# Performance work log

Hardware: AMD Instinct MI355X
Metric: run time of the kernel (lower is better)

## Reference

```python
import jax, jax.numpy as jnp
import numpy as np

C = 512
NUM_HEADS = 8
HEAD_DIM = C // NUM_HEADS  # 64
BN_EPS = 1e-5


def setup_inputs() -> dict:
    key = jax.random.key(0)
    ks = jax.random.split(key, 12)
    B, H, W = 8, 32, 32
    s = 0.02
    return {
        "x": jax.random.normal(ks[0], (B, C, H, W), dtype=jnp.float32),
        "gamma": jnp.ones((C,), jnp.float32),
        "beta": jnp.zeros((C,), jnp.float32),
        "rmean": jnp.zeros((C,), jnp.float32),
        "rvar": jnp.ones((C,), jnp.float32),
        "wq": jax.random.normal(ks[1], (C, C), jnp.float32) * s,
        "bq": jnp.zeros((C,), jnp.float32),
        "wk": jax.random.normal(ks[2], (C, C), jnp.float32) * s,
        "bk": jnp.zeros((C,), jnp.float32),
        "wv": jax.random.normal(ks[3], (C, C), jnp.float32) * s,
        "bv": jnp.zeros((C,), jnp.float32),
        "wp": jax.random.normal(ks[4], (C, C), jnp.float32) * s,
        "bp": jnp.zeros((C,), jnp.float32),
    }


def _conv1x1(w, b, h):
    # 1x1 conv == per-pixel dense: (O,C) x (B,C,H,W) -> (B,O,H,W)
    return jnp.einsum('oc,bchw->bohw', w, h) + b[None, :, None, None]


def reference(x, gamma, beta, rmean, rvar, wq, bq, wk, bk, wv, bv, wp, bp):
    B, Cc, H, W = x.shape
    N = H * W
    # BatchNorm2d (eval mode, running stats)
    inv = gamma / jnp.sqrt(rvar + BN_EPS)
    h = x * inv[None, :, None, None] + (beta - rmean * inv)[None, :, None, None]
    q = _conv1x1(wq, bq, h).reshape(B, NUM_HEADS, HEAD_DIM, N)
    k = _conv1x1(wk, bk, h).reshape(B, NUM_HEADS, HEAD_DIM, N)
    v = _conv1x1(wv, bv, h).reshape(B, NUM_HEADS, HEAD_DIM, N)
    scale = 1.0 / np.sqrt(HEAD_DIM).astype(np.float32)
    attn = jnp.einsum('bhdn,bhdm->bhnm', q, k) * scale  # [B,heads,N,N]
    attn = jnp.clip(attn, -50.0, 50.0)
    attn = jax.nn.softmax(attn, axis=-1)
    out = jnp.einsum('bhnm,bhdm->bhdn', attn, v).reshape(B, Cc, H, W)
    out = _conv1x1(wp, bp, out)
    return x + out
```

## Files before the change

kernel.cpp:

```cpp
#include <hip/hip_runtime.h>
#include <stdint.h>

#define C_DIM 512
#define NHEADS 8
#define HDIM 64
#define BATCH 8
#define NPIX 1024
#define Q_PRESCALE 0.18033688011112042f

typedef __bf16 bf16x8 __attribute__((ext_vector_type(8)));
typedef float f32x4 __attribute__((ext_vector_type(4)));
typedef float f32x16 __attribute__((ext_vector_type(16)));

__device__ __forceinline__ unsigned short f2bf(float f) {
  union { float f; unsigned u; } v; v.f = f;
  unsigned r = v.u + 0x7fffu + ((v.u >> 16) & 1u);
  return (unsigned short)(r >> 16);
}

__device__ __forceinline__ void gl_lds16(const void* g, void* l) {
  __builtin_amdgcn_global_load_lds(
      (__attribute__((address_space(1))) void*)g,
      (__attribute__((address_space(3))) void*)l,
      16, 0, 0);
}

__global__ __launch_bounds__(256) void k_prep(const float* __restrict__ wq,
                                              const float* __restrict__ wk,
                                              const float* __restrict__ wv,
                                              const float* __restrict__ wp,
                                              unsigned short* __restrict__ wbf) {
  const int n = C_DIM * C_DIM;
  for (int i = blockIdx.x * blockDim.x + threadIdx.x; i < 4 * n;
       i += gridDim.x * blockDim.x) {
    const float* src = (i < n) ? wq : (i < 2 * n) ? wk : (i < 3 * n) ? wv : wp;
    wbf[i] = f2bf(src[i & (n - 1)]);
  }
}

__global__ __launch_bounds__(256) void k_bnT(const float* __restrict__ x,
                                             const float* __restrict__ gamma,
                                             const float* __restrict__ beta,
                                             const float* __restrict__ rmean,
                                             const float* __restrict__ rvar,
                                             unsigned short* __restrict__ hbT) {
  __shared__ unsigned short tile[64][72];
  const int b = blockIdx.z, c0 = blockIdx.y * 64, n0 = blockIdx.x * 64;
  const int t = threadIdx.x;
#pragma unroll
  for (int it = 0; it < 4; ++it) {
    int c = it * 16 + (t >> 4);
    int n = (t & 15) * 4;
    const float4 v = *(const float4*)&x[((size_t)b * C_DIM + c0 + c) * NPIX + n0 + n];
    int cc = c0 + c;
    float inv = gamma[cc] * rsqrtf(rvar[cc] + 1e-5f);
    float add = beta[cc] - rmean[cc] * inv;
    tile[c][n + 0] = f2bf(v.x * inv + add);
    tile[c][n + 1] = f2bf(v.y * inv + add);
    tile[c][n + 2] = f2bf(v.z * inv + add);
    tile[c][n + 3] = f2bf(v.w * inv + add);
  }
  __syncthreads();
#pragma unroll
  for (int it = 0; it < 2; ++it) {
    int n = it * 32 + (t >> 3);
    int cj = (t & 7) * 8;
    unsigned short tmp[8];
#pragma unroll
    for (int u = 0; u < 8; ++u) tmp[u] = tile[cj + u][n];
    uint4 pk;
    pk.x = (unsigned)tmp[0] | ((unsigned)tmp[1] << 16);
    pk.y = (unsigned)tmp[2] | ((unsigned)tmp[3] << 16);
    pk.z = (unsigned)tmp[4] | ((unsigned)tmp[5] << 16);
    pk.w = (unsigned)tmp[6] | ((unsigned)tmp[7] << 16);
    *(uint4*)&hbT[((size_t)b * NPIX + n0 + n) * C_DIM + c0 + cj] = pk;
  }
}

__global__ __launch_bounds__(256) void k_qkv(const unsigned short* __restrict__ wbf,
                                             const float* __restrict__ bq,
                                             const float* __restrict__ bk,
                                             const float* __restrict__ bv,
                                             const unsigned short* __restrict__ hbT,
                                             unsigned short* __restrict__ QT,
                                             unsigned short* __restrict__ KT,
                                             unsigned short* __restrict__ Vb) {
  __shared__ unsigned short Atile[128 * 32];
  __shared__ unsigned short Btile[128 * 32];
  const int which = blockIdx.z >> 3;
  const int b = blockIdx.z & 7;
  const int m0 = blockIdx.y * 128, n0 = blockIdx.x * 128;
  const unsigned short* W = wbf + (size_t)which * C_DIM * C_DIM;
  const int t = threadIdx.x, wave = t >> 6, lane = t & 63;
  const int wr = wave >> 1, wc = wave & 1;
  f32x4 acc[4][4] = {};

  const int st_row = lane >> 2;
  const int st_col = (((lane & 3) ^ ((lane >> 3) & 3))) * 8;

  for (int k0 = 0; k0 < C_DIM; k0 += 32) {
    __syncthreads();
#pragma unroll
    for (int it = 0; it < 2; ++it) {
      int q = wave + 4 * it;
      int row = q * 16 + st_row;
      gl_lds16(&W[(size_t)(m0 + row) * C_DIM + k0 + st_col], &Atile[q * 512]);
      gl_lds16(&hbT[((size_t)b * NPIX + n0 + row) * C_DIM + k0 + st_col], &Btile[q * 512]);
    }
    __syncthreads();
    bf16x8 af[4], bfr[4];
#pragma unroll
    for (int i = 0; i < 4; ++i) {
      int row = wr * 64 + i * 16 + (lane & 15);
      af[i] = *(const bf16x8*)&Atile[row * 32 + (((lane >> 4) ^ ((row >> 1) & 3)) * 8)];
    }
#pragma unroll
    for (int j = 0; j < 4; ++j) {
      int row = wc * 64 + j * 16 + (lane & 15);
      bfr[j] = *(const bf16x8*)&Btile[row * 32 + (((lane >> 4) ^ ((row >> 1) & 3)) * 8)];
    }
#pragma unroll
    for (int i = 0; i < 4; ++i)
#pragma unroll
      for (int j = 0; j < 4; ++j)
        acc[i][j] = __builtin_amdgcn_mfma_f32_16x16x32_bf16(af[i], bfr[j], acc[i][j], 0, 0, 0);
  }

  const float* bias = (which == 0) ? bq : (which == 1) ? bk : bv;
  if (which < 2) {
    unsigned short* T = (which == 0) ? QT : KT;
    const float qs = (which == 0) ? Q_PRESCALE : 1.0f;
#pragma unroll
    for (int i = 0; i < 4; ++i) {
      int o = m0 + wr * 64 + i * 16 + (lane >> 4) * 4;
      float b0 = bias[o + 0], b1 = bias[o + 1], b2 = bias[o + 2], b3 = bias[o + 3];
#pragma unroll
      for (int j = 0; j < 4; ++j) {
        int n = n0 + wc * 64 + j * 16 + (lane & 15);
        ushort4 pk;
        pk.x = f2bf((acc[i][j][0] + b0) * qs);
        pk.y = f2bf((acc[i][j][1] + b1) * qs);
        pk.z = f2bf((acc[i][j][2] + b2) * qs);
        pk.w = f2bf((acc[i][j][3] + b3) * qs);
        *(ushort4*)&T[((size_t)b * NPIX + n) * C_DIM + o] = pk;
      }
    }
  } else {
#pragma unroll
    for (int i = 0; i < 4; ++i) {
      int o = m0 + wr * 64 + i * 16 + (lane >> 4) * 4;
#pragma unroll
      for (int j = 0; j < 4; ++j) {
        int n = n0 + wc * 64 + j * 16 + (lane & 15);
#pragma unroll
        for (int r = 0; r < 4; ++r)
          Vb[((size_t)b * C_DIM + o + r) * NPIX + n] = f2bf(acc[i][j][r] + bias[o + r]);
      }
    }
  }
}

__global__ __launch_bounds__(256) void k_attn(const unsigned short* __restrict__ QT,
                                              const unsigned short* __restrict__ KT,
                                              const unsigned short* __restrict__ Vb,
                                              unsigned short* __restrict__ OA,
                                              unsigned short* __restrict__ OB,
                                              float* __restrict__ rs) {
  __shared__ unsigned short Ks[2][64 * 64];
  __shared__ unsigned short Vs[2][64 * 64];

  const int bid = blockIdx.x;
  const int b = bid & 7, h = (bid >> 3) & 7, qt = (bid >> 6) & 7, ks = bid >> 9;
  const int n0 = qt * 128;
  const int kbase0 = ks * 512;
  const int lane = threadIdx.x & 63, wave = threadIdx.x >> 6;
  const int l31 = lane & 31, hi = lane >> 5;

  bf16x8 qf[4];
  {
    const unsigned short* qbase =
        QT + ((size_t)b * NPIX + n0 + wave * 32 + l31) * C_DIM + h * HDIM + hi * 8;
#pragma unroll
    for (int kk = 0; kk < 4; ++kk) qf[kk] = *(const bf16x8*)(qbase + kk * 16);
  }

  union { unsigned u[4]; bf16x8 v; } ones;
  ones.u[0] = 0x3F803F80u; ones.u[1] = 0x3F803F80u;
  ones.u[2] = 0x3F803F80u; ones.u[3] = 0x3F803F80u;

  auto stage = [&](int buf, int tile) {
    const int m0 = kbase0 + tile * 64;
#pragma unroll
    for (int it = 0; it < 2; ++it) {
      int rb = it * 32 + wave * 8;
      int row = rb + (lane >> 3);
      int srcc = ((lane & 7) ^ (row & 7)) * 8;
      gl_lds16(&KT[((size_t)b * NPIX + m0 + row) * C_DIM + h * HDIM + srcc],
               &Ks[buf][rb * 64]);
      int srck = ((lane & 7) ^ (row & 7)) * 8;
      gl_lds16(&Vb[((size_t)b * C_DIM + h * HDIM + row) * NPIX + m0 + srck],
               &Vs[buf][rb * 64]);
    }
  };

  f32x16 oacc[2] = {};
  f32x16 rsacc = {};

  stage(0, 0);
  __syncthreads();

  for (int tile = 0; tile < 8; ++tile) {
    const int cur = tile & 1;
    if (tile < 7) stage(cur ^ 1, tile + 1);

#pragma unroll
    for (int kt = 0; kt < 2; ++kt) {
      f32x16 s = {};
#pragma unroll
      for (int kk = 0; kk < 4; ++kk) {
        int row = kt * 32 + l31;
        int phys = (kk * 2 + hi) ^ (row & 7);
        bf16x8 kf = *(const bf16x8*)&Ks[cur][row * 64 + phys * 8];
        s = __builtin_amdgcn_mfma_f32_32x32x16_bf16(kf, qf[kk], s, 0, 0, 0);
      }
      unsigned w[8];
#pragma unroll
      for (int r2 = 0; r2 < 8; ++r2) {
        float e0 = exp2f(s[2 * r2]);
        float e1 = exp2f(s[2 * r2 + 1]);
        asm("v_cvt_pk_bf16_f32 %0, %1, %2" : "=v"(w[r2]) : "v"(e0), "v"(e1));
      }
      asm volatile("v_permlane32_swap_b32 %0, %1" : "+v"(w[0]), "+v"(w[2]));
      asm volatile("v_permlane32_swap_b32 %0, %1" : "+v"(w[1]), "+v"(w[3]));
      asm volatile("v_permlane32_swap_b32 %0, %1" : "+v"(w[4]), "+v"(w[6]));
      asm volatile("v_permlane32_swap_b32 %0, %1" : "+v"(w[5]), "+v"(w[7]));
      union U8 { unsigned u[4]; bf16x8 v; };
      U8 pa0, pa1;
      pa0.u[0] = w[0]; pa0.u[1] = w[1]; pa0.u[2] = w[2]; pa0.u[3] = w[3];
      pa1.u[0] = w[4]; pa1.u[1] = w[5]; pa1.u[2] = w[6]; pa1.u[3] = w[7];
      rsacc = __builtin_amdgcn_mfma_f32_32x32x16_bf16(pa0.v, ones.v, rsacc, 0, 0, 0);
      rsacc = __builtin_amdgcn_mfma_f32_32x32x16_bf16(pa1.v, ones.v, rsacc, 0, 0, 0);
#pragma unroll
      for (int dt = 0; dt < 2; ++dt) {
        int d = dt * 32 + l31;
        bf16x8 v0 = *(const bf16x8*)&Vs[cur][d * 64 + (((kt * 4 + hi) ^ (d & 7)) * 8)];
        bf16x8 v1 = *(const bf16x8*)&Vs[cur][d * 64 + (((kt * 4 + 2 + hi) ^ (d & 7)) * 8)];
        oacc[dt] = __builtin_amdgcn_mfma_f32_32x32x16_bf16(pa0.v, v0, oacc[dt], 0, 0, 0);
        oacc[dt] = __builtin_amdgcn_mfma_f32_32x32x16_bf16(pa1.v, v1, oacc[dt], 0, 0, 0);
      }
    }
    __syncthreads();
  }

  float inv[16];
#pragma unroll
  for (int r = 0; r < 16; ++r) inv[r] = 1.0f / rsacc[r];

  unsigned short* obuf = (ks == 0) ? OA : OB;
  __bf16* obase = (__bf16*)(obuf + ((size_t)b * NPIX + n0 + wave * 32) * C_DIM +
                            h * HDIM + l31);
#pragma unroll
  for (int dt = 0; dt < 2; ++dt)
#pragma unroll
    for (int r = 0; r < 16; ++r) {
      int q = (r & 3) + 8 * (r >> 2) + 4 * hi;
      obase[(size_t)q * C_DIM + dt * 32] = (__bf16)(oacc[dt][r] * inv[r]);
    }
  if (l31 == 0) {
    float* rbase = rs + (((size_t)ks * 8 + b) * 8 + h) * NPIX + n0 + wave * 32;
#pragma unroll
    for (int r = 0; r < 16; ++r)
      rbase[(r & 3) + 8 * (r >> 2) + 4 * hi] = rsacc[r];
  }
}

__global__ __launch_bounds__(256) void k_comb(const unsigned short* OA,
                                              const unsigned short* OB,
                                              const float* __restrict__ rs,
                                              unsigned short* AOT) {
  int i = blockIdx.x * 256 + threadIdx.x;
  int b = i >> 16;
  int rem = i & 65535;
  int n = rem >> 6;
  int c8 = rem & 63;
  int h = c8 >> 3;
  size_t off = ((size_t)b * NPIX + n) * C_DIM + c8 * 8;
  float rsA = rs[(((size_t)0 * 8 + b) * 8 + h) * NPIX + n];
  float rsB = rs[(((size_t)1 * 8 + b) * 8 + h) * NPIX + n];
  float sA = rsA / (rsA + rsB);
  float sB = 1.0f - sA;
  uint4 a = *(const uint4*)(OA + off);
  uint4 bb = *(const uint4*)(OB + off);
  const unsigned* au = (const unsigned*)&a;
  const unsigned* bu = (const unsigned*)&bb;
  uint4 o;
  unsigned* ou = (unsigned*)&o;
#pragma unroll
  for (int j = 0; j < 4; ++j) {
    float a0, a1, b0, b1;
    union { unsigned u; float f; } t;
    t.u = (au[j] & 0xFFFFu) << 16; a0 = t.f;
    t.u = au[j] & 0xFFFF0000u;     a1 = t.f;
    t.u = (bu[j] & 0xFFFFu) << 16; b0 = t.f;
    t.u = bu[j] & 0xFFFF0000u;     b1 = t.f;
    float o0 = sA * a0 + sB * b0;
    float o1 = sA * a1 + sB * b1;
    unsigned pk;
    asm("v_cvt_pk_bf16_f32 %0, %1, %2" : "=v"(pk) : "v"(o0), "v"(o1));
    ou[j] = pk;
  }
  *(uint4*)(AOT + off) = o;
}

__global__ __launch_bounds__(256) void k_proj(const unsigned short* __restrict__ Wp,
                                              const float* __restrict__ bp,
                                              const unsigned short* __restrict__ AOT,
                                              const float* __restrict__ x,
                                              float* __restrict__ out) {
  __shared__ unsigned short Atile[128 * 32];
  __shared__ unsigned short Btile[128 * 32];
  const int b = blockIdx.z;
  const int m0 = blockIdx.y * 128, n0 = blockIdx.x * 128;
  const int t = threadIdx.x, wave = t >> 6, lane = t & 63;
  const int wr = wave >> 1, wc = wave & 1;
  f32x4 acc[4][4] = {};
  const int st_row = lane >> 2;
  const int st_col = (((lane & 3) ^ ((lane >> 3) & 3))) * 8;

  for (int k0 = 0; k0 < C_DIM; k0 += 32) {
    __syncthreads();
#pragma unroll
    for (int it = 0; it < 2; ++it) {
      int q = wave + 4 * it;
      int row = q * 16 + st_row;
      gl_lds16(&Wp[(size_t)(m0 + row) * C_DIM + k0 + st_col], &Atile[q * 512]);
      gl_lds16(&AOT[((size_t)b * NPIX + n0 + row) * C_DIM + k0 + st_col], &Btile[q * 512]);
    }
    __syncthreads();
    bf16x8 af[4], bfr[4];
#pragma unroll
    for (int i = 0; i < 4; ++i) {
      int row = wr * 64 + i * 16 + (lane & 15);
      af[i] = *(const bf16x8*)&Atile[row * 32 + (((lane >> 4) ^ ((row >> 1) & 3)) * 8)];
    }
#pragma unroll
    for (int j = 0; j < 4; ++j) {
      int row = wc * 64 + j * 16 + (lane & 15);
      bfr[j] = *(const bf16x8*)&Btile[row * 32 + (((lane >> 4) ^ ((row >> 1) & 3)) * 8)];
    }
#pragma unroll
    for (int i = 0; i < 4; ++i)
#pragma unroll
      for (int j = 0; j < 4; ++j)
        acc[i][j] = __builtin_amdgcn_mfma_f32_16x16x32_bf16(af[i], bfr[j], acc[i][j], 0, 0, 0);
  }

#pragma unroll
  for (int i = 0; i < 4; ++i) {
    int o = m0 + wr * 64 + i * 16 + (lane >> 4) * 4;
    float b0 = bp[o + 0], b1 = bp[o + 1], b2 = bp[o + 2], b3 = bp[o + 3];
#pragma unroll
    for (int j = 0; j < 4; ++j) {
      int n = n0 + wc * 64 + j * 16 + (lane & 15);
      size_t base = ((size_t)b * C_DIM + o) * NPIX + n;
      out[base + 0 * NPIX] = acc[i][j][0] + b0 + x[base + 0 * NPIX];
      out[base + 1 * NPIX] = acc[i][j][1] + b1 + x[base + 1 * NPIX];
      out[base + 2 * NPIX] = acc[i][j][2] + b2 + x[base + 2 * NPIX];
      out[base + 3 * NPIX] = acc[i][j][3] + b3 + x[base + 3 * NPIX];
    }
  }
}

extern "C" void kernel_launch(void* const* d_in, const int* in_sizes, int n_in,
                              void* d_out, int out_size, void* d_ws, size_t ws_size,
                              hipStream_t stream) {
  (void)in_sizes; (void)n_in; (void)out_size; (void)ws_size;
  const float* x     = (const float*)d_in[0];
  const float* gamma = (const float*)d_in[1];
  const float* beta  = (const float*)d_in[2];
  const float* rmean = (const float*)d_in[3];
  const float* rvar  = (const float*)d_in[4];
  const float* wq    = (const float*)d_in[5];
  const float* bq    = (const float*)d_in[6];
  const float* wk    = (const float*)d_in[7];
  const float* bk    = (const float*)d_in[8];
  const float* wv    = (const float*)d_in[9];
  const float* bv    = (const float*)d_in[10];
  const float* wp    = (const float*)d_in[11];
  const float* bp    = (const float*)d_in[12];

  unsigned short* ws  = (unsigned short*)d_ws;
  const size_t WSZ    = (size_t)C_DIM * C_DIM;
  const size_t BIG    = (size_t)BATCH * NPIX * C_DIM;
  unsigned short* wbf = ws;
  unsigned short* hbT = wbf + 4 * WSZ;
  unsigned short* QT  = hbT + BIG;
  unsigned short* KT  = QT + BIG;
  unsigned short* Vb  = KT + BIG;
  unsigned short* AOT = Vb + BIG;
  float*          rs  = (float*)(AOT + BIG);

  k_prep<<<dim3(512), dim3(256), 0, stream>>>(wq, wk, wv, wp, wbf);
  k_bnT<<<dim3(16, 8, 8), dim3(256), 0, stream>>>(x, gamma, beta, rmean, rvar, hbT);
  k_qkv<<<dim3(8, 4, 24), dim3(256), 0, stream>>>(wbf, bq, bk, bv, hbT, QT, KT, Vb);
  k_attn<<<dim3(1024), dim3(256), 0, stream>>>(QT, KT, Vb, AOT, hbT, rs);
  k_comb<<<dim3(2048), dim3(256), 0, stream>>>(AOT, hbT, rs, AOT);
  k_proj<<<dim3(8, 4, 8), dim3(256), 0, stream>>>(wbf + 3 * WSZ, bp, AOT, x, (float*)d_out);
}
```

Before: 176.4 us.

## Deepen attention K/V pipeline to triple buffering and widen QKV GEMM K-step

The attention kernel moves from double to triple-buffered K/V tiles in LDS. It prefetches two tiles ahead and uses partial vmcnt waits with raw barriers, so loads for later tiles stay in flight while the current tile is computed. The QKV GEMM now stages a 64-wide K slice per iteration with an XOR swizzle, which halves the number of barrier pairs. The cost is more LDS per block, which may lower occupancy, plus correctness risk from the hand-tuned waitcnt counts.

```diff
diff --git a/kernel.cpp b/kernel.cpp
--- a/kernel.cpp
+++ b/kernel.cpp
@@ -85,8 +85,8 @@
                                              unsigned short* __restrict__ QT,
                                              unsigned short* __restrict__ KT,
                                              unsigned short* __restrict__ Vb) {
-  __shared__ unsigned short Atile[128 * 32];
-  __shared__ unsigned short Btile[128 * 32];
+  __shared__ unsigned short Atile[128 * 64];
+  __shared__ unsigned short Btile[128 * 64];
   const int which = blockIdx.z >> 3;
   const int b = blockIdx.z & 7;
   const int m0 = blockIdx.y * 128, n0 = blockIdx.x * 128;
@@ -95,35 +95,39 @@
   const int wr = wave >> 1, wc = wave & 1;
   f32x4 acc[4][4] = {};
 
-  const int st_row = lane >> 2;
-  const int st_col = (((lane & 3) ^ ((lane >> 3) & 3))) * 8;
-
-  for (int k0 = 0; k0 < C_DIM; k0 += 32) {
+  for (int k0 = 0; k0 < C_DIM; k0 += 64) {
     __syncthreads();
 #pragma unroll
-    for (int it = 0; it < 2; ++it) {
-      int q = wave + 4 * it;
-      int row = q * 16 + st_row;
-      gl_lds16(&W[(size_t)(m0 + row) * C_DIM + k0 + st_col], &Atile[q * 512]);
-      gl_lds16(&hbT[((size_t)b * NPIX + n0 + row) * C_DIM + k0 + st_col], &Btile[q * 512]);
+    for (int s = 0; s < 4; ++s) {
+      int row = s * 32 + wave * 8 + (lane >> 3);
+      int srcc = ((lane & 7) ^ (row & 7)) * 8;
+      gl_lds16(&W[(size_t)(m0 + row) * C_DIM + k0 + srcc],
+               &Atile[(s * 32 + wave * 8) * 64]);
+      gl_lds16(&hbT[((size_t)b * NPIX + n0 + row) * C_DIM + k0 + srcc],
+               &Btile[(s * 32 + wave * 8) * 64]);
     }
     __syncthreads();
-    bf16x8 af[4], bfr[4];
-#pragma unroll
-    for (int i = 0; i < 4; ++i) {
-      int row = wr * 64 + i * 16 + (lane & 15);
-      af[i] = *(const bf16x8*)&Atile[row * 32 + (((lane >> 4) ^ ((row >> 1) & 3)) * 8)];
-    }
-#pragma unroll
-    for (int j = 0; j < 4; ++j) {
-      int row = wc * 64 + j * 16 + (lane & 15);
-      bfr[j] = *(const bf16x8*)&Btile[row * 32 + (((lane >> 4) ^ ((row >> 1) & 3)) * 8)];
-    }
-#pragma unroll
-    for (int i = 0; i < 4; ++i)
-#pragma unroll
-      for (int j = 0; j < 4; ++j)
-        acc[i][j] = __builtin_amdgcn_mfma_f32_16x16x32_bf16(af[i], bfr[j], acc[i][j], 0, 0, 0);
+#pragma unroll
+    for (int ks2 = 0; ks2 < 2; ++ks2) {
+      bf16x8 af[4], bfr[4];
+#pragma unroll
+      for (int i = 0; i < 4; ++i) {
+        int row = wr * 64 + i * 16 + (lane & 15);
+        int phys = (ks2 * 4 + (lane >> 4)) ^ (row & 7);
+        af[i] = *(const bf16x8*)&Atile[row * 64 + phys * 8];
+      }
+#pragma unroll
+      for (int j = 0; j < 4; ++j) {
+        int row = wc * 64 + j * 16 + (lane & 15);
+        int phys = (ks2 * 4 + (lane >> 4)) ^ (row & 7);
+        bfr[j] = *(const bf16x8*)&Btile[row * 64 + phys * 8];
+      }
+#pragma unroll
+      for (int i = 0; i < 4; ++i)
+#pragma unroll
+        for (int j = 0; j < 4; ++j)
+          acc[i][j] = __builtin_amdgcn_mfma_f32_16x16x32_bf16(af[i], bfr[j], acc[i][j], 0, 0, 0);
+    }
   }
 
   const float* bias = (which == 0) ? bq : (which == 1) ? bk : bv;
@@ -166,8 +170,8 @@
                                               unsigned short* __restrict__ OA,
                                               unsigned short* __restrict__ OB,
                                               float* __restrict__ rs) {
-  __shared__ unsigned short Ks[2][64 * 64];
-  __shared__ unsigned short Vs[2][64 * 64];
+  __shared__ unsigned short Ks[3][64 * 64];
+  __shared__ unsigned short Vs[3][64 * 64];
 
   const int bid = blockIdx.x;
   const int b = bid & 7, h = (bid >> 3) & 7, qt = (bid >> 6) & 7, ks = bid >> 9;
@@ -197,8 +201,7 @@
       int srcc = ((lane & 7) ^ (row & 7)) * 8;
       gl_lds16(&KT[((size_t)b * NPIX + m0 + row) * C_DIM + h * HDIM + srcc],
                &Ks[buf][rb * 64]);
-      int srck = ((lane & 7) ^ (row & 7)) * 8;
-      gl_lds16(&Vb[((size_t)b * C_DIM + h * HDIM + row) * NPIX + m0 + srck],
+      gl_lds16(&Vb[((size_t)b * C_DIM + h * HDIM + row) * NPIX + m0 + srcc],
                &Vs[buf][rb * 64]);
     }
   };
@@ -207,11 +210,15 @@
   f32x16 rsacc = {};
 
   stage(0, 0);
-  __syncthreads();
-
+  stage(1, 1);
+  asm volatile("s_waitcnt vmcnt(4)" ::: "memory");
+  __builtin_amdgcn_s_barrier();
+  __builtin_amdgcn_sched_barrier(0);
+
+#pragma unroll
   for (int tile = 0; tile < 8; ++tile) {
-    const int cur = tile & 1;
-    if (tile < 7) stage(cur ^ 1, tile + 1);
+    const int cur = tile % 3;
+    if (tile < 6) stage((tile + 2) % 3, tile + 2);
 
 #pragma unroll
     for (int kt = 0; kt < 2; ++kt) {
@@ -249,7 +256,16 @@
         oacc[dt] = __builtin_amdgcn_mfma_f32_32x32x16_bf16(pa1.v, v1, oacc[dt], 0, 0, 0);
       }
     }
-    __syncthreads();
+
+    if (tile < 6) {
+      asm volatile("s_waitcnt vmcnt(4)" ::: "memory");
+      __builtin_amdgcn_s_barrier();
+      __builtin_amdgcn_sched_barrier(0);
+    } else if (tile == 6) {
+      asm volatile("s_waitcnt vmcnt(0)" ::: "memory");
+      __builtin_amdgcn_s_barrier();
+      __builtin_amdgcn_sched_barrier(0);
+    }
   }
 
   float inv[16];
```

After: 173.1 us. About the same (-1.9%).
